# Kernel tuning notes

Measured on AMD Instinct MI355X. Metric: run time of the kernel, lower is better.

## Reference

```python
import jax, jax.numpy as jnp
import numpy as np


def _conv1x1(x, W, b):
    # x: [b,c,h,w], W: [out,in], b: [out]
    return jnp.einsum('oi,bihw->bohw', W, x) + b[None, :, None, None]


def setup_inputs() -> dict:
    key = jax.random.key(0)
    ks = jax.random.split(key, 8)
    B, C, H, W = 4, 256, 64, 64
    s = 1.0 / np.sqrt(C)
    return {
        'x1': jax.random.normal(ks[0], (B, C, H, W), jnp.float32),
        'x2': jax.random.normal(ks[1], (B, C, H, W), jnp.float32),
        'Wq': jax.random.normal(ks[2], (C, C), jnp.float32) * s,
        'bq': jax.random.normal(ks[3], (C,), jnp.float32) * 0.01,
        'Wk': jax.random.normal(ks[4], (C, C), jnp.float32) * s,
        'bk': jax.random.normal(ks[5], (C,), jnp.float32) * 0.01,
        'Wv': jax.random.normal(ks[6], (C, C), jnp.float32) * s,
        'bv': jax.random.normal(ks[7], (C,), jnp.float32) * 0.01,
    }


def reference(x1, x2, Wq, bq, Wk, bk, Wv, bv):
    b, c, h, w = x1.shape
    n = h * w
    q = _conv1x1(x1, Wq, bq).reshape(b, c, n)   # [b,c,n]
    k = _conv1x1(x2, Wk, bk).reshape(b, c, n)   # [b,c,n]
    v = _conv1x1(x2, Wv, bv).reshape(b, c, n)   # [b,c,n]
    # scores[b,i,j] = sum_c q[b,c,i] * k[b,c,j]; softmax over j (last dim)
    scores = jnp.einsum('bci,bcj->bij', q, k)
    attn = jax.nn.softmax(scores, axis=-1)      # [b,n,n]
    # out[b,c,i] = sum_j v[b,c,j] * attn[b,i,j]  (v @ attn^T)
    out = jnp.einsum('bcj,bij->bci', v, attn)
    return out.reshape(b, c, h, w)
```

## Files before the change

### kernel.cpp

```cpp
#include <hip/hip_runtime.h>

#define BATCH 4
#define CDIM 256
#define NDIM 4096
#define SPLITS 4
#define KSPLIT (NDIM / SPLITS)
#define JT 32
#define NTILES (KSPLIT / JT)

typedef unsigned short u16;
typedef unsigned int u32;
typedef _Float16 f16;
typedef __attribute__((ext_vector_type(8))) _Float16 half8;
typedef __attribute__((ext_vector_type(4))) float floatx4;

__device__ __forceinline__ void load_lds_128(const void* g, void* l) {
  __builtin_amdgcn_global_load_lds(
      (const __attribute__((address_space(1))) u32*)g,
      (__attribute__((address_space(3))) u32*)l, 16, 0, 0);
}

__global__ __launch_bounds__(256) void prep_w_k(
    const float* __restrict__ wq, const float* __restrict__ wk,
    const float* __restrict__ wv, f16* __restrict__ whq,
    f16* __restrict__ whk, f16* __restrict__ whv) {
  const int gid = blockIdx.x * 256 + threadIdx.x;
  const int a = gid >> 13;
  const int r = gid & 8191;
  const float* src = (a == 0) ? wq : ((a == 1) ? wk : wv);
  f16* dst = (a == 0) ? whq : ((a == 1) ? whk : whv);
  float4 v0 = *(const float4*)(src + r * 8);
  float4 v1 = *(const float4*)(src + r * 8 + 4);
  half8 h;
  h[0] = (f16)v0.x; h[1] = (f16)v0.y; h[2] = (f16)v0.z; h[3] = (f16)v0.w;
  h[4] = (f16)v1.x; h[5] = (f16)v1.y; h[6] = (f16)v1.z; h[7] = (f16)v1.w;
  *(half8*)(dst + r * 8) = h;
}

__global__ __launch_bounds__(256) void transpose_k(
    const float* __restrict__ x1, const float* __restrict__ x2,
    f16* __restrict__ xt1, f16* __restrict__ xt2) {
  __shared__ __align__(16) float tile[64 * 68];
  const int z = blockIdx.z;
  const float* src = (z & 1) ? x2 : x1;
  f16* dst = (z & 1) ? xt2 : xt1;
  const int b = z >> 1;
  src += (size_t)b * CDIM * NDIM;
  dst += (size_t)b * NDIM * CDIM;
  const int n0 = blockIdx.x * 64, c0 = blockIdx.y * 64;
  const int t = threadIdx.x;
#pragma unroll
  for (int it = 0; it < 4; ++it) {
    int chunk = t + it * 256;
    int row = chunk >> 4;
    int col4 = (chunk & 15) << 2;
    float4 v = *(const float4*)(src + (size_t)(c0 + row) * NDIM + (n0 + col4));
    *(float4*)&tile[row * 68 + col4] = v;
  }
  __syncthreads();
#pragma unroll
  for (int it = 0; it < 2; ++it) {
    int task = t + it * 256;
    int nl = task >> 3;
    int cb = (task & 7) << 3;
    half8 h;
#pragma unroll
    for (int j = 0; j < 8; ++j) h[j] = (f16)tile[(cb + j) * 68 + nl];
    *(half8*)(dst + (size_t)(n0 + nl) * CDIM + (c0 + cb)) = h;
  }
}

__global__ __launch_bounds__(256, 2) void proj_qk_k(
    const f16* __restrict__ xt1, const f16* __restrict__ xt2,
    const f16* __restrict__ whq, const float* __restrict__ bq,
    const f16* __restrict__ whk, const float* __restrict__ bk,
    f16* __restrict__ qt, f16* __restrict__ kt) {
  const int z = blockIdx.z;
  const int which = z & 1, b = z >> 1;
  const f16* xt = which ? xt2 : xt1;
  const f16* w = which ? whk : whq;
  const float* bias = which ? bk : bq;
  f16* outp = which ? kt : qt;
  xt += (size_t)b * NDIM * CDIM;
  outp += (size_t)b * NDIM * CDIM;
  const int c0 = blockIdx.x * 128, i0 = blockIdx.y * 128;
  const int tid = threadIdx.x;
  const int wave = tid >> 6, lane = tid & 63, l16 = lane & 15, grp = lane >> 4;
  const int wi = (wave & 1) * 64, wc = (wave >> 1) * 64;
  floatx4 acc[4][4];
#pragma unroll
  for (int mb = 0; mb < 4; ++mb)
#pragma unroll
    for (int nb = 0; nb < 4; ++nb) acc[mb][nb] = (floatx4){0.f, 0.f, 0.f, 0.f};
#pragma unroll
  for (int ks = 0; ks < 8; ++ks) {
    const int kofs = ks * 32 + grp * 8;
    half8 a[4], bb[4];
#pragma unroll
    for (int mb = 0; mb < 4; ++mb)
      a[mb] = *(const half8*)(xt + (size_t)(i0 + wi + mb * 16 + l16) * CDIM + kofs);
#pragma unroll
    for (int nb = 0; nb < 4; ++nb)
      bb[nb] = *(const half8*)(w + (size_t)(c0 + wc + nb * 16 + l16) * CDIM + kofs);
#pragma unroll
    for (int mb = 0; mb < 4; ++mb)
#pragma unroll
      for (int nb = 0; nb < 4; ++nb)
        acc[mb][nb] = __builtin_amdgcn_mfma_f32_16x16x32_f16(a[mb], bb[nb], acc[mb][nb], 0, 0, 0);
  }
#pragma unroll
  for (int nb = 0; nb < 4; ++nb) {
    const int c = c0 + wc + nb * 16 + l16;
    const float bv = bias[c];
#pragma unroll
    for (int mb = 0; mb < 4; ++mb) {
      const int ibase = i0 + wi + mb * 16 + grp * 4;
#pragma unroll
      for (int r = 0; r < 4; ++r)
        outp[(size_t)(ibase + r) * CDIM + c] = (f16)(acc[mb][nb][r] + bv);
    }
  }
}

__global__ __launch_bounds__(256, 2) void proj_v_k(
    const f16* __restrict__ xt2, const f16* __restrict__ whv,
    const float* __restrict__ bv, f16* __restrict__ vsout) {
  const int b = blockIdx.z;
  const f16* xt = xt2 + (size_t)b * NDIM * CDIM;
  f16* outp = vsout + (size_t)b * CDIM * NDIM;
  const int c0 = blockIdx.x * 128, j0 = blockIdx.y * 128;
  const int tid = threadIdx.x;
  const int wave = tid >> 6, lane = tid & 63, l16 = lane & 15, grp = lane >> 4;
  const int wc = (wave & 1) * 64, wj = (wave >> 1) * 64;
  floatx4 acc[4][4];
#pragma unroll
  for (int mb = 0; mb < 4; ++mb)
#pragma unroll
    for (int nb = 0; nb < 4; ++nb) acc[mb][nb] = (floatx4){0.f, 0.f, 0.f, 0.f};
#pragma unroll
  for (int ks = 0; ks < 8; ++ks) {
    const int kofs = ks * 32 + grp * 8;
    half8 a[4], bb[4];
#pragma unroll
    for (int mb = 0; mb < 4; ++mb)
      a[mb] = *(const half8*)(whv + (size_t)(c0 + wc + mb * 16 + l16) * CDIM + kofs);
#pragma unroll
    for (int nb = 0; nb < 4; ++nb)
      bb[nb] = *(const half8*)(xt + (size_t)(j0 + wj + nb * 16 + l16) * CDIM + kofs);
#pragma unroll
    for (int mb = 0; mb < 4; ++mb)
#pragma unroll
      for (int nb = 0; nb < 4; ++nb)
        acc[mb][nb] = __builtin_amdgcn_mfma_f32_16x16x32_f16(a[mb], bb[nb], acc[mb][nb], 0, 0, 0);
  }
#pragma unroll
  for (int mb = 0; mb < 4; ++mb)
#pragma unroll
    for (int r = 0; r < 4; ++r) {
      const int c = c0 + wc + mb * 16 + grp * 4 + r;
      const float bvv = bv[c];
#pragma unroll
      for (int nb = 0; nb < 4; ++nb) {
        const int j = j0 + wj + nb * 16 + l16;
        outp[(size_t)c * NDIM + j] = (f16)(acc[mb][nb][r] + bvv);
      }
    }
}

__global__ __launch_bounds__(256, 2) void flash_k(
    const f16* __restrict__ qt, const f16* __restrict__ kt,
    const f16* __restrict__ vs, f16* __restrict__ pO,
    float* __restrict__ pm, float* __restrict__ pl) {
  __shared__ __align__(16) u16 smem[25600];
  const int bx = blockIdx.x;
  const int c16 = bx & 15;
  const int b = c16 >> 2, s = c16 & 3;
  const int i0 = (bx >> 4) * 128;
  const int jwin = s * KSPLIT;
  const f16* Q = qt + (size_t)b * NDIM * CDIM;
  const f16* K = kt + (size_t)b * NDIM * CDIM;
  const f16* V = vs + (size_t)b * CDIM * NDIM;
  const int tid = threadIdx.x;
  const int wave = tid >> 6, lane = tid & 63, l16 = lane & 15, grp = lane >> 4;
  u16* bK = smem;
  u16* bV = smem + 8192;
  float* Pw = (float*)(smem + 16384) + wave * (32 * 36);

  half8 qf[2][8];
#pragma unroll
  for (int mb = 0; mb < 2; ++mb)
#pragma unroll
    for (int ks = 0; ks < 8; ++ks)
      qf[mb][ks] = *(const half8*)(Q + (size_t)(i0 + wave * 32 + mb * 16 + l16) * CDIM +
                                   ks * 32 + grp * 8);

  floatx4 O[2][16];
#pragma unroll
  for (int mb = 0; mb < 2; ++mb)
#pragma unroll
    for (int cb = 0; cb < 16; ++cb) O[mb][cb] = (floatx4){0.f, 0.f, 0.f, 0.f};
  float m_[2][4], l_[2][4];
#pragma unroll
  for (int mb = 0; mb < 2; ++mb)
#pragma unroll
    for (int r = 0; r < 4; ++r) { m_[mb][r] = -1e30f; l_[mb][r] = 0.f; }

  for (int tt = 0; tt < NTILES; ++tt) {
    const int j0 = jwin + tt * JT;
    __syncthreads();
#pragma unroll
    for (int it = 0; it < 4; ++it) {
      const int row = wave * 8 + it * 2 + (lane >> 5);
      const int p = lane & 31;
      const int g = p ^ (row & 7);
      load_lds_128(K + (size_t)(j0 + row) * CDIM + g * 8, &bK[(wave * 8 + it * 2) * 256]);
    }
#pragma unroll
    for (int it = 0; it < 4; ++it) {
      const int c = wave * 64 + it * 16 + (lane >> 2);
      const int p = lane & 3;
      const int g = p ^ (c & 3);
      load_lds_128(V + (size_t)c * NDIM + j0 + g * 8, &bV[(wave * 64 + it * 16) * 32]);
    }
    __syncthreads();

    floatx4 S[2][2];
#pragma unroll
    for (int mb = 0; mb < 2; ++mb)
#pragma unroll
      for (int jb = 0; jb < 2; ++jb) S[mb][jb] = (floatx4){0.f, 0.f, 0.f, 0.f};
#pragma unroll
    for (int ks = 0; ks < 8; ++ks) {
      const int chunk = ks * 4 + grp;
#pragma unroll
      for (int jb = 0; jb < 2; ++jb) {
        const int row = jb * 16 + l16;
        half8 kf = *(const half8*)&bK[row * 256 + ((chunk ^ (row & 7)) << 3)];
        S[0][jb] = __builtin_amdgcn_mfma_f32_16x16x32_f16(qf[0][ks], kf, S[0][jb], 0, 0, 0);
        S[1][jb] = __builtin_amdgcn_mfma_f32_16x16x32_f16(qf[1][ks], kf, S[1][jb], 0, 0, 0);
      }
    }

#pragma unroll
    for (int mb = 0; mb < 2; ++mb) {
      float mnew[4];
#pragma unroll
      for (int r = 0; r < 4; ++r) mnew[r] = fmaxf(S[mb][0][r], S[mb][1][r]);
#pragma unroll
      for (int mask = 1; mask < 16; mask <<= 1)
#pragma unroll
        for (int r = 0; r < 4; ++r) mnew[r] = fmaxf(mnew[r], __shfl_xor(mnew[r], mask, 64));
      float alpha[4], rs[4];
#pragma unroll
      for (int r = 0; r < 4; ++r) {
        const float mt = fmaxf(m_[mb][r], mnew[r]);
        alpha[r] = __expf(m_[mb][r] - mt);
        m_[mb][r] = mt;
      }
#pragma unroll
      for (int r = 0; r < 4; ++r) {
        S[mb][0][r] = __expf(S[mb][0][r] - m_[mb][r]);
        S[mb][1][r] = __expf(S[mb][1][r] - m_[mb][r]);
        rs[r] = S[mb][0][r] + S[mb][1][r];
      }
#pragma unroll
      for (int mask = 1; mask < 16; mask <<= 1)
#pragma unroll
        for (int r = 0; r < 4; ++r) rs[r] += __shfl_xor(rs[r], mask, 64);
#pragma unroll
      for (int r = 0; r < 4; ++r) l_[mb][r] = l_[mb][r] * alpha[r] + rs[r];
#pragma unroll
      for (int cb = 0; cb < 16; ++cb)
#pragma unroll
        for (int r = 0; r < 4; ++r) O[mb][cb][r] *= alpha[r];
    }

#pragma unroll
    for (int mb = 0; mb < 2; ++mb)
#pragma unroll
      for (int jb = 0; jb < 2; ++jb)
#pragma unroll
        for (int r = 0; r < 4; ++r)
          Pw[(mb * 16 + grp * 4 + r) * 36 + jb * 16 + l16] = S[mb][jb][r];
    half8 pa[2];
#pragma unroll
    for (int mb = 0; mb < 2; ++mb) {
      floatx4 u0 = *(const floatx4*)&Pw[(mb * 16 + l16) * 36 + grp * 8];
      floatx4 u1 = *(const floatx4*)&Pw[(mb * 16 + l16) * 36 + grp * 8 + 4];
      half8 h;
      h[0] = (f16)u0[0]; h[1] = (f16)u0[1]; h[2] = (f16)u0[2]; h[3] = (f16)u0[3];
      h[4] = (f16)u1[0]; h[5] = (f16)u1[1]; h[6] = (f16)u1[2]; h[7] = (f16)u1[3];
      pa[mb] = h;
    }

#pragma unroll
    for (int cb = 0; cb < 16; ++cb) {
      const int c = cb * 16 + l16;
      half8 vf = *(const half8*)&bV[c * 32 + ((grp ^ (c & 3)) << 3)];
      O[0][cb] = __builtin_amdgcn_mfma_f32_16x16x32_f16(pa[0], vf, O[0][cb], 0, 0, 0);
      O[1][cb] = __builtin_amdgcn_mfma_f32_16x16x32_f16(pa[1], vf, O[1][cb], 0, 0, 0);
    }
  }

#pragma unroll
  for (int quarter = 0; quarter < 4; ++quarter) {
    __syncthreads();
    float* sO = (float*)smem;
#pragma unroll
    for (int mb = 0; mb < 2; ++mb)
#pragma unroll
      for (int cb4 = 0; cb4 < 4; ++cb4) {
        const int cb = quarter * 4 + cb4;
        const int cl = cb4 * 16 + l16;
        const int i = wave * 32 + mb * 16 + grp * 4;
        *(floatx4*)&sO[cl * 132 + i] = O[mb][cb];
      }
    __syncthreads();
    const size_t obase = ((size_t)(b * SPLITS + s) * CDIM + quarter * 64) * NDIM + i0;
#pragma unroll
    for (int it = 0; it < 4; ++it) {
      const int task = tid + it * 256;
      const int cl = task >> 4, p = (task & 15) * 8;
      floatx4 v0 = *(const floatx4*)&sO[cl * 132 + p];
      floatx4 v1 = *(const floatx4*)&sO[cl * 132 + p + 4];
      half8 h;
      h[0] = (f16)v0[0]; h[1] = (f16)v0[1]; h[2] = (f16)v0[2]; h[3] = (f16)v0[3];
      h[4] = (f16)v1[0]; h[5] = (f16)v1[1]; h[6] = (f16)v1[2]; h[7] = (f16)v1[3];
      *(half8*)(pO + obase + (size_t)cl * NDIM + p) = h;
    }
  }
  if (l16 == 0) {
    const int base = (b * SPLITS + s) * NDIM + i0;
#pragma unroll
    for (int mb = 0; mb < 2; ++mb)
#pragma unroll
      for (int r = 0; r < 4; ++r) {
        const int i = wave * 32 + mb * 16 + grp * 4 + r;
        pm[base + i] = m_[mb][r];
        pl[base + i] = l_[mb][r];
      }
  }
}

__global__ __launch_bounds__(256) void combine_k(
    const f16* __restrict__ pO, const float* __restrict__ pm,
    const float* __restrict__ pl, float* __restrict__ out) {
  __shared__ float su[SPLITS][64];
  const int b = blockIdx.x >> 6;
  const int i0 = (blockIdx.x & 63) * 64;
  const int t = threadIdx.x;
  if (t < 64) {
    const int i = i0 + t;
    float mv[SPLITS], w[SPLITS];
    float M = -3e38f;
#pragma unroll
    for (int s = 0; s < SPLITS; ++s) {
      mv[s] = pm[(b * SPLITS + s) * NDIM + i];
      M = fmaxf(M, mv[s]);
    }
    float L = 0.f;
#pragma unroll
    for (int s = 0; s < SPLITS; ++s) {
      w[s] = __expf(mv[s] - M);
      L += pl[(b * SPLITS + s) * NDIM + i] * w[s];
    }
    const float invL = 1.0f / L;
#pragma unroll
    for (int s = 0; s < SPLITS; ++s) su[s][t] = w[s] * invL;
  }
  __syncthreads();
#pragma unroll
  for (int it = 0; it < 8; ++it) {
    const int task = t + it * 256;
    const int c = task >> 3, p = (task & 7) * 8;
    float acc[8] = {0.f, 0.f, 0.f, 0.f, 0.f, 0.f, 0.f, 0.f};
#pragma unroll
    for (int s = 0; s < SPLITS; ++s) {
      const f16* src = pO + ((size_t)(b * SPLITS + s) * CDIM + c) * NDIM + i0 + p;
      half8 h = *(const half8*)src;
#pragma unroll
      for (int j = 0; j < 8; ++j) acc[j] += su[s][p + j] * (float)h[j];
    }
    float* dst = out + ((size_t)b * CDIM + c) * NDIM + i0 + p;
    float4 lo = {acc[0], acc[1], acc[2], acc[3]};
    float4 hi = {acc[4], acc[5], acc[6], acc[7]};
    *(float4*)dst = lo;
    *(float4*)(dst + 4) = hi;
  }
}

extern "C" void kernel_launch(void* const* d_in, const int* in_sizes, int n_in,
                              void* d_out, int out_size, void* d_ws, size_t ws_size,
                              hipStream_t stream) {
  const float* x1 = (const float*)d_in[0];
  const float* x2 = (const float*)d_in[1];
  const float* Wq = (const float*)d_in[2];
  const float* bq = (const float*)d_in[3];
  const float* Wk = (const float*)d_in[4];
  const float* bk = (const float*)d_in[5];
  const float* Wv = (const float*)d_in[6];
  const float* bv = (const float*)d_in[7];
  float* out = (float*)d_out;
  char* ws = (char*)d_ws;
  f16* qtp = (f16*)(ws + 0);
  f16* ktp = (f16*)(ws + 8388608);
  f16* vsp = (f16*)(ws + 16777216);
  f16* xt1 = (f16*)(ws + 25165824);
  f16* xt2 = (f16*)(ws + 33554432);
  f16* whq = (f16*)(ws + 41943040);
  f16* whk = whq + CDIM * CDIM;
  f16* whv = whk + CDIM * CDIM;
  f16* pO = (f16*)(ws + 25165824);
  float* pm = (float*)(ws + 58720256);
  float* pl = (float*)(ws + 58982400);

  prep_w_k<<<dim3(96), dim3(256), 0, stream>>>(Wq, Wk, Wv, whq, whk, whv);
  transpose_k<<<dim3(NDIM / 64, CDIM / 64, 2 * BATCH), dim3(256), 0, stream>>>(x1, x2, xt1, xt2);
  proj_qk_k<<<dim3(2, 32, 2 * BATCH), dim3(256), 0, stream>>>(xt1, xt2, whq, bq, whk, bk, qtp, ktp);
  proj_v_k<<<dim3(2, 32, BATCH), dim3(256), 0, stream>>>(xt2, whv, bv, vsp);
  flash_k<<<dim3(512), dim3(256), 0, stream>>>(qtp, ktp, vsp, pO, pm, pl);
  combine_k<<<dim3(256), dim3(256), 0, stream>>>(pO, pm, pl, out);
}
```

Before: 310.3 us.

## Enlarge flash query tile, double-buffer K/V loads, defer row-sum reduction

The flash kernel now handles 256 query rows per block (64 per wave), so each K/V tile staged in LDS is reused across twice as many rows, and the grid is halved to 256 blocks at one block per CU. K/V tiles are double-buffered, with the next tile's async global-to-LDS load issued before computing on the current one, removing one barrier per iteration. Q fragments are no longer held in registers and are reloaded from global memory each tile. The softmax row-sum shuffle reduction is deferred to after the loop, and O rescaling is skipped when no row maximum increases. The costs are higher register pressure, lower occupancy, and repeated Q traffic through cache.

```diff
diff --git a/kernel.cpp b/kernel.cpp
--- a/kernel.cpp
+++ b/kernel.cpp
@@ -167,82 +167,94 @@
     }
 }
 
-__global__ __launch_bounds__(256, 2) void flash_k(
+__global__ __launch_bounds__(256, 1) void flash_k(
     const f16* __restrict__ qt, const f16* __restrict__ kt,
     const f16* __restrict__ vs, f16* __restrict__ pO,
     float* __restrict__ pm, float* __restrict__ pl) {
-  __shared__ __align__(16) u16 smem[25600];
+  __shared__ __align__(16) u16 smem[51200];
   const int bx = blockIdx.x;
   const int c16 = bx & 15;
   const int b = c16 >> 2, s = c16 & 3;
-  const int i0 = (bx >> 4) * 128;
+  const int i0 = (bx >> 4) * 256;
   const int jwin = s * KSPLIT;
-  const f16* Q = qt + (size_t)b * NDIM * CDIM;
   const f16* K = kt + (size_t)b * NDIM * CDIM;
   const f16* V = vs + (size_t)b * CDIM * NDIM;
   const int tid = threadIdx.x;
   const int wave = tid >> 6, lane = tid & 63, l16 = lane & 15, grp = lane >> 4;
-  u16* bK = smem;
-  u16* bV = smem + 8192;
-  float* Pw = (float*)(smem + 16384) + wave * (32 * 36);
-
-  half8 qf[2][8];
-#pragma unroll
-  for (int mb = 0; mb < 2; ++mb)
-#pragma unroll
-    for (int ks = 0; ks < 8; ++ks)
-      qf[mb][ks] = *(const half8*)(Q + (size_t)(i0 + wave * 32 + mb * 16 + l16) * CDIM +
-                                   ks * 32 + grp * 8);
-
-  floatx4 O[2][16];
-#pragma unroll
-  for (int mb = 0; mb < 2; ++mb)
+  const int wq = wave * 64;
+  const f16* Qw = qt + (size_t)b * NDIM * CDIM + (size_t)(i0 + wq + l16) * CDIM + grp * 8;
+
+  float* Pw = (float*)(smem + 32768) + wave * (64 * 36);
+
+  floatx4 O[4][16];
+#pragma unroll
+  for (int mb = 0; mb < 4; ++mb)
 #pragma unroll
     for (int cb = 0; cb < 16; ++cb) O[mb][cb] = (floatx4){0.f, 0.f, 0.f, 0.f};
-  float m_[2][4], l_[2][4];
-#pragma unroll
-  for (int mb = 0; mb < 2; ++mb)
-#pragma unroll
-    for (int r = 0; r < 4; ++r) { m_[mb][r] = -1e30f; l_[mb][r] = 0.f; }
+  float m_[4][4], lsum[4][4];
+#pragma unroll
+  for (int mb = 0; mb < 4; ++mb)
+#pragma unroll
+    for (int r = 0; r < 4; ++r) { m_[mb][r] = -1e30f; lsum[mb][r] = 0.f; }
+
+  const int kr2 = lane >> 5, kp = lane & 31;
+  const int vrow = lane >> 2, vp = lane & 3;
+
+#define STAGE(J0, BUF)                                                         \
+  {                                                                            \
+    u16* sK = smem + (BUF) * 16384;                                            \
+    u16* sV = sK + 8192;                                                       \
+    _Pragma("unroll") for (int it = 0; it < 4; ++it) {                         \
+      const int row = wave * 8 + it * 2 + kr2;                                 \
+      const int g = kp ^ (row & 7);                                            \
+      load_lds_128(K + (size_t)((J0) + row) * CDIM + g * 8,                    \
+                   &sK[(wave * 8 + it * 2) * 256]);                            \
+    }                                                                          \
+    _Pragma("unroll") for (int it = 0; it < 4; ++it) {                         \
+      const int c = wave * 64 + it * 16 + vrow;                                \
+      const int g = vp ^ ((c >> 2) & 3);                                       \
+      load_lds_128(V + (size_t)c * NDIM + (J0) + g * 8,                        \
+                   &sV[(wave * 64 + it * 16) * 32]);                           \
+    }                                                                          \
+  }
+
+  STAGE(jwin, 0)
 
   for (int tt = 0; tt < NTILES; ++tt) {
-    const int j0 = jwin + tt * JT;
+    u16* bK = smem + (tt & 1) * 16384;
+    u16* bV = bK + 8192;
     __syncthreads();
-#pragma unroll
-    for (int it = 0; it < 4; ++it) {
-      const int row = wave * 8 + it * 2 + (lane >> 5);
-      const int p = lane & 31;
-      const int g = p ^ (row & 7);
-      load_lds_128(K + (size_t)(j0 + row) * CDIM + g * 8, &bK[(wave * 8 + it * 2) * 256]);
-    }
-#pragma unroll
-    for (int it = 0; it < 4; ++it) {
-      const int c = wave * 64 + it * 16 + (lane >> 2);
-      const int p = lane & 3;
-      const int g = p ^ (c & 3);
-      load_lds_128(V + (size_t)c * NDIM + j0 + g * 8, &bV[(wave * 64 + it * 16) * 32]);
-    }
-    __syncthreads();
-
-    floatx4 S[2][2];
-#pragma unroll
-    for (int mb = 0; mb < 2; ++mb)
+    if (tt + 1 < NTILES) STAGE(jwin + (tt + 1) * JT, (tt + 1) & 1)
+
+    floatx4 S[4][2];
+#pragma unroll
+    for (int mb = 0; mb < 4; ++mb)
 #pragma unroll
       for (int jb = 0; jb < 2; ++jb) S[mb][jb] = (floatx4){0.f, 0.f, 0.f, 0.f};
 #pragma unroll
-    for (int ks = 0; ks < 8; ++ks) {
-      const int chunk = ks * 4 + grp;
-#pragma unroll
-      for (int jb = 0; jb < 2; ++jb) {
-        const int row = jb * 16 + l16;
-        half8 kf = *(const half8*)&bK[row * 256 + ((chunk ^ (row & 7)) << 3)];
-        S[0][jb] = __builtin_amdgcn_mfma_f32_16x16x32_f16(qf[0][ks], kf, S[0][jb], 0, 0, 0);
-        S[1][jb] = __builtin_amdgcn_mfma_f32_16x16x32_f16(qf[1][ks], kf, S[1][jb], 0, 0, 0);
-      }
-    }
-
-#pragma unroll
-    for (int mb = 0; mb < 2; ++mb) {
+    for (int half = 0; half < 2; ++half) {
+      half8 qh[4][4];
+#pragma unroll
+      for (int mb = 0; mb < 4; ++mb)
+#pragma unroll
+        for (int kk = 0; kk < 4; ++kk)
+          qh[mb][kk] = *(const half8*)(Qw + (size_t)(mb * 16) * CDIM + (half * 4 + kk) * 32);
+#pragma unroll
+      for (int kk = 0; kk < 4; ++kk) {
+        const int chunk = (half * 4 + kk) * 4 + grp;
+#pragma unroll
+        for (int jb = 0; jb < 2; ++jb) {
+          const int row = jb * 16 + l16;
+          half8 kf = *(const half8*)&bK[row * 256 + ((chunk ^ (row & 7)) << 3)];
+#pragma unroll
+          for (int mb = 0; mb < 4; ++mb)
+            S[mb][jb] = __builtin_amdgcn_mfma_f32_16x16x32_f16(qh[mb][kk], kf, S[mb][jb], 0, 0, 0);
+        }
+      }
+    }
+
+#pragma unroll
+    for (int mb = 0; mb < 4; ++mb) {
       float mnew[4];
 #pragma unroll
       for (int r = 0; r < 4; ++r) mnew[r] = fmaxf(S[mb][0][r], S[mb][1][r]);
@@ -250,41 +262,39 @@
       for (int mask = 1; mask < 16; mask <<= 1)
 #pragma unroll
         for (int r = 0; r < 4; ++r) mnew[r] = fmaxf(mnew[r], __shfl_xor(mnew[r], mask, 64));
-      float alpha[4], rs[4];
-#pragma unroll
-      for (int r = 0; r < 4; ++r) {
-        const float mt = fmaxf(m_[mb][r], mnew[r]);
-        alpha[r] = __expf(m_[mb][r] - mt);
-        m_[mb][r] = mt;
+      bool upd = false;
+#pragma unroll
+      for (int r = 0; r < 4; ++r) upd = upd || (mnew[r] > m_[mb][r]);
+      if (__any(upd)) {
+        float alpha[4];
+#pragma unroll
+        for (int r = 0; r < 4; ++r) {
+          const float mt = fmaxf(m_[mb][r], mnew[r]);
+          alpha[r] = __expf(m_[mb][r] - mt);
+          m_[mb][r] = mt;
+          lsum[mb][r] *= alpha[r];
+        }
+#pragma unroll
+        for (int cb = 0; cb < 16; ++cb)
+#pragma unroll
+          for (int r = 0; r < 4; ++r) O[mb][cb][r] *= alpha[r];
       }
 #pragma unroll
       for (int r = 0; r < 4; ++r) {
         S[mb][0][r] = __expf(S[mb][0][r] - m_[mb][r]);
         S[mb][1][r] = __expf(S[mb][1][r] - m_[mb][r]);
-        rs[r] = S[mb][0][r] + S[mb][1][r];
-      }
-#pragma unroll
-      for (int mask = 1; mask < 16; mask <<= 1)
-#pragma unroll
-        for (int r = 0; r < 4; ++r) rs[r] += __shfl_xor(rs[r], mask, 64);
-#pragma unroll
-      for (int r = 0; r < 4; ++r) l_[mb][r] = l_[mb][r] * alpha[r] + rs[r];
-#pragma unroll
-      for (int cb = 0; cb < 16; ++cb)
-#pragma unroll
-        for (int r = 0; r < 4; ++r) O[mb][cb][r] *= alpha[r];
-    }
-
-#pragma unroll
-    for (int mb = 0; mb < 2; ++mb)
+        lsum[mb][r] += S[mb][0][r] + S[mb][1][r];
+      }
 #pragma unroll
       for (int jb = 0; jb < 2; ++jb)
 #pragma unroll
         for (int r = 0; r < 4; ++r)
           Pw[(mb * 16 + grp * 4 + r) * 36 + jb * 16 + l16] = S[mb][jb][r];
-    half8 pa[2];
-#pragma unroll
-    for (int mb = 0; mb < 2; ++mb) {
+    }
+
+    half8 pa[4];
+#pragma unroll
+    for (int mb = 0; mb < 4; ++mb) {
       floatx4 u0 = *(const floatx4*)&Pw[(mb * 16 + l16) * 36 + grp * 8];
       floatx4 u1 = *(const floatx4*)&Pw[(mb * 16 + l16) * 36 + grp * 8 + 4];
       half8 h;
@@ -296,10 +306,29 @@
 #pragma unroll
     for (int cb = 0; cb < 16; ++cb) {
       const int c = cb * 16 + l16;
-      half8 vf = *(const half8*)&bV[c * 32 + ((grp ^ (c & 3)) << 3)];
-      O[0][cb] = __builtin_amdgcn_mfma_f32_16x16x32_f16(pa[0], vf, O[0][cb], 0, 0, 0);
-      O[1][cb] = __builtin_amdgcn_mfma_f32_16x16x32_f16(pa[1], vf, O[1][cb], 0, 0, 0);
-    }
+      half8 vf = *(const half8*)&bV[c * 32 + ((grp ^ ((c >> 2) & 3)) << 3)];
+#pragma unroll
+      for (int mb = 0; mb < 4; ++mb)
+        O[mb][cb] = __builtin_amdgcn_mfma_f32_16x16x32_f16(pa[mb], vf, O[mb][cb], 0, 0, 0);
+    }
+  }
+
+#pragma unroll
+  for (int mask = 1; mask < 16; mask <<= 1)
+#pragma unroll
+    for (int mb = 0; mb < 4; ++mb)
+#pragma unroll
+      for (int r = 0; r < 4; ++r) lsum[mb][r] += __shfl_xor(lsum[mb][r], mask, 64);
+  if (l16 == 0) {
+    const int base = (b * SPLITS + s) * NDIM + i0;
+#pragma unroll
+    for (int mb = 0; mb < 4; ++mb)
+#pragma unroll
+      for (int r = 0; r < 4; ++r) {
+        const int i = wq + mb * 16 + grp * 4 + r;
+        pm[base + i] = m_[mb][r];
+        pl[base + i] = lsum[mb][r];
+      }
   }
 
 #pragma unroll
@@ -307,38 +336,27 @@
     __syncthreads();
     float* sO = (float*)smem;
 #pragma unroll
-    for (int mb = 0; mb < 2; ++mb)
+    for (int mb = 0; mb < 4; ++mb)
 #pragma unroll
       for (int cb4 = 0; cb4 < 4; ++cb4) {
         const int cb = quarter * 4 + cb4;
         const int cl = cb4 * 16 + l16;
-        const int i = wave * 32 + mb * 16 + grp * 4;
-        *(floatx4*)&sO[cl * 132 + i] = O[mb][cb];
+        const int i = wq + mb * 16 + grp * 4;
+        *(floatx4*)&sO[cl * 260 + i] = O[mb][cb];
       }
     __syncthreads();
     const size_t obase = ((size_t)(b * SPLITS + s) * CDIM + quarter * 64) * NDIM + i0;
 #pragma unroll
-    for (int it = 0; it < 4; ++it) {
+    for (int it = 0; it < 8; ++it) {
       const int task = tid + it * 256;
-      const int cl = task >> 4, p = (task & 15) * 8;
-      floatx4 v0 = *(const floatx4*)&sO[cl * 132 + p];
-      floatx4 v1 = *(const floatx4*)&sO[cl * 132 + p + 4];
+      const int cl = task >> 5, p = (task & 31) * 8;
+      floatx4 v0 = *(const floatx4*)&sO[cl * 260 + p];
+      floatx4 v1 = *(const floatx4*)&sO[cl * 260 + p + 4];
       half8 h;
       h[0] = (f16)v0[0]; h[1] = (f16)v0[1]; h[2] = (f16)v0[2]; h[3] = (f16)v0[3];
       h[4] = (f16)v1[0]; h[5] = (f16)v1[1]; h[6] = (f16)v1[2]; h[7] = (f16)v1[3];
       *(half8*)(pO + obase + (size_t)cl * NDIM + p) = h;
     }
-  }
-  if (l16 == 0) {
-    const int base = (b * SPLITS + s) * NDIM + i0;
-#pragma unroll
-    for (int mb = 0; mb < 2; ++mb)
-#pragma unroll
-      for (int r = 0; r < 4; ++r) {
-        const int i = wave * 32 + mb * 16 + grp * 4 + r;
-        pm[base + i] = m_[mb][r];
-        pl[base + i] = l_[mb][r];
-      }
   }
 }
 
@@ -418,6 +436,6 @@
   transpose_k<<<dim3(NDIM / 64, CDIM / 64, 2 * BATCH), dim3(256), 0, stream>>>(x1, x2, xt1, xt2);
   proj_qk_k<<<dim3(2, 32, 2 * BATCH), dim3(256), 0, stream>>>(xt1, xt2, whq, bq, whk, bk, qtp, ktp);
   proj_v_k<<<dim3(2, 32, BATCH), dim3(256), 0, stream>>>(xt2, whv, bv, vsp);
-  flash_k<<<dim3(512), dim3(256), 0, stream>>>(qtp, ktp, vsp, pO, pm, pl);
+  flash_k<<<dim3(256), dim3(256), 0, stream>>>(qtp, ktp, vsp, pO, pm, pl);
   combine_k<<<dim3(256), dim3(256), 0, stream>>>(pO, pm, pl, out);
 }
```

Result: slower. 707.3 us (+127.9%).

## Double-buffer K/V tiles and transpose PV MFMA for row-local softmax

Applied to the files above, without the earlier changes.

Splits LDS into two K/V buffers so the next tile's global-to-LDS loads are issued while the current tile is computed, leaving one barrier per iteration. Swaps the MFMA operands in the P·V product so each lane holds a full query row. This lets the online softmax use per-lane max and sum with only two cross-lane shuffles, and the O rescale is skipped when no alpha in the wave is below one. The LDS-staged epilogue is replaced with direct strided f16 stores, which are less coalesced. LDS use per block also grows.

```diff
diff --git a/kernel.cpp b/kernel.cpp
--- a/kernel.cpp
+++ b/kernel.cpp
@@ -171,7 +171,7 @@
     const f16* __restrict__ qt, const f16* __restrict__ kt,
     const f16* __restrict__ vs, f16* __restrict__ pO,
     float* __restrict__ pm, float* __restrict__ pl) {
-  __shared__ __align__(16) u16 smem[25600];
+  __shared__ __align__(16) u16 smem[32768 + 4608];
   const int bx = blockIdx.x;
   const int c16 = bx & 15;
   const int b = c16 >> 2, s = c16 & 3;
@@ -182,9 +182,7 @@
   const f16* V = vs + (size_t)b * CDIM * NDIM;
   const int tid = threadIdx.x;
   const int wave = tid >> 6, lane = tid & 63, l16 = lane & 15, grp = lane >> 4;
-  u16* bK = smem;
-  u16* bV = smem + 8192;
-  float* Pw = (float*)(smem + 16384) + wave * (32 * 36);
+  float* Pw = (float*)(smem + 32768) + wave * (16 * 36);
 
   half8 qf[2][8];
 #pragma unroll
@@ -199,30 +197,37 @@
   for (int mb = 0; mb < 2; ++mb)
 #pragma unroll
     for (int cb = 0; cb < 16; ++cb) O[mb][cb] = (floatx4){0.f, 0.f, 0.f, 0.f};
-  float m_[2][4], l_[2][4];
-#pragma unroll
-  for (int mb = 0; mb < 2; ++mb)
-#pragma unroll
-    for (int r = 0; r < 4; ++r) { m_[mb][r] = -1e30f; l_[mb][r] = 0.f; }
+  float m_[2] = {-1e30f, -1e30f};
+  float lsum[2] = {0.f, 0.f};
+
+  const int kr2 = lane >> 5, kp = lane & 31;
+  const int vrow = lane >> 2, vp = lane & 3;
+
+#define STAGE(J0, BUF)                                                         \
+  {                                                                            \
+    u16* sK = smem + (BUF) * 16384;                                            \
+    u16* sV = sK + 8192;                                                       \
+    _Pragma("unroll") for (int it = 0; it < 4; ++it) {                         \
+      const int row = wave * 8 + it * 2 + kr2;                                 \
+      const int g = kp ^ (row & 7);                                            \
+      load_lds_128(K + (size_t)((J0) + row) * CDIM + g * 8,                    \
+                   &sK[(wave * 8 + it * 2) * 256]);                            \
+    }                                                                          \
+    _Pragma("unroll") for (int it = 0; it < 4; ++it) {                         \
+      const int c = wave * 64 + it * 16 + vrow;                                \
+      const int g = vp ^ ((c >> 2) & 3);                                       \
+      load_lds_128(V + (size_t)c * NDIM + (J0) + g * 8,                        \
+                   &sV[(wave * 64 + it * 16) * 32]);                           \
+    }                                                                          \
+  }
+
+  STAGE(jwin, 0)
 
   for (int tt = 0; tt < NTILES; ++tt) {
-    const int j0 = jwin + tt * JT;
     __syncthreads();
-#pragma unroll
-    for (int it = 0; it < 4; ++it) {
-      const int row = wave * 8 + it * 2 + (lane >> 5);
-      const int p = lane & 31;
-      const int g = p ^ (row & 7);
-      load_lds_128(K + (size_t)(j0 + row) * CDIM + g * 8, &bK[(wave * 8 + it * 2) * 256]);
-    }
-#pragma unroll
-    for (int it = 0; it < 4; ++it) {
-      const int c = wave * 64 + it * 16 + (lane >> 2);
-      const int p = lane & 3;
-      const int g = p ^ (c & 3);
-      load_lds_128(V + (size_t)c * NDIM + j0 + g * 8, &bV[(wave * 64 + it * 16) * 32]);
-    }
-    __syncthreads();
+    if (tt + 1 < NTILES) STAGE(jwin + (tt + 1) * JT, (tt + 1) & 1)
+    u16* bK = smem + (tt & 1) * 16384;
+    u16* bV = bK + 8192;
 
     floatx4 S[2][2];
 #pragma unroll
@@ -241,104 +246,80 @@
       }
     }
 
+    float alpha[2];
+    half8 pa[2];
 #pragma unroll
     for (int mb = 0; mb < 2; ++mb) {
-      float mnew[4];
-#pragma unroll
-      for (int r = 0; r < 4; ++r) mnew[r] = fmaxf(S[mb][0][r], S[mb][1][r]);
-#pragma unroll
-      for (int mask = 1; mask < 16; mask <<= 1)
-#pragma unroll
-        for (int r = 0; r < 4; ++r) mnew[r] = fmaxf(mnew[r], __shfl_xor(mnew[r], mask, 64));
-      float alpha[4], rs[4];
-#pragma unroll
-      for (int r = 0; r < 4; ++r) {
-        const float mt = fmaxf(m_[mb][r], mnew[r]);
-        alpha[r] = __expf(m_[mb][r] - mt);
-        m_[mb][r] = mt;
-      }
-#pragma unroll
-      for (int r = 0; r < 4; ++r) {
-        S[mb][0][r] = __expf(S[mb][0][r] - m_[mb][r]);
-        S[mb][1][r] = __expf(S[mb][1][r] - m_[mb][r]);
-        rs[r] = S[mb][0][r] + S[mb][1][r];
-      }
-#pragma unroll
-      for (int mask = 1; mask < 16; mask <<= 1)
-#pragma unroll
-        for (int r = 0; r < 4; ++r) rs[r] += __shfl_xor(rs[r], mask, 64);
-#pragma unroll
-      for (int r = 0; r < 4; ++r) l_[mb][r] = l_[mb][r] * alpha[r] + rs[r];
-#pragma unroll
-      for (int cb = 0; cb < 16; ++cb)
-#pragma unroll
-        for (int r = 0; r < 4; ++r) O[mb][cb][r] *= alpha[r];
-    }
-
-#pragma unroll
-    for (int mb = 0; mb < 2; ++mb)
 #pragma unroll
       for (int jb = 0; jb < 2; ++jb)
 #pragma unroll
         for (int r = 0; r < 4; ++r)
-          Pw[(mb * 16 + grp * 4 + r) * 36 + jb * 16 + l16] = S[mb][jb][r];
-    half8 pa[2];
-#pragma unroll
-    for (int mb = 0; mb < 2; ++mb) {
-      floatx4 u0 = *(const floatx4*)&Pw[(mb * 16 + l16) * 36 + grp * 8];
-      floatx4 u1 = *(const floatx4*)&Pw[(mb * 16 + l16) * 36 + grp * 8 + 4];
+          Pw[(grp * 4 + r) * 36 + jb * 16 + l16] = S[mb][jb][r];
+      floatx4 u0 = *(const floatx4*)&Pw[l16 * 36 + grp * 8];
+      floatx4 u1 = *(const floatx4*)&Pw[l16 * 36 + grp * 8 + 4];
+      float mx = fmaxf(fmaxf(fmaxf(u0[0], u0[1]), fmaxf(u0[2], u0[3])),
+                       fmaxf(fmaxf(u1[0], u1[1]), fmaxf(u1[2], u1[3])));
+      mx = fmaxf(mx, __shfl_xor(mx, 16, 64));
+      mx = fmaxf(mx, __shfl_xor(mx, 32, 64));
+      const float mnew = fmaxf(m_[mb], mx);
+      alpha[mb] = __expf(m_[mb] - mnew);
+      m_[mb] = mnew;
+      float pe[8];
+#pragma unroll
+      for (int j = 0; j < 4; ++j) pe[j] = __expf(u0[j] - mnew);
+#pragma unroll
+      for (int j = 0; j < 4; ++j) pe[4 + j] = __expf(u1[j] - mnew);
+      const float ps = ((pe[0] + pe[1]) + (pe[2] + pe[3])) +
+                       ((pe[4] + pe[5]) + (pe[6] + pe[7]));
+      lsum[mb] = lsum[mb] * alpha[mb] + ps;
       half8 h;
-      h[0] = (f16)u0[0]; h[1] = (f16)u0[1]; h[2] = (f16)u0[2]; h[3] = (f16)u0[3];
-      h[4] = (f16)u1[0]; h[5] = (f16)u1[1]; h[6] = (f16)u1[2]; h[7] = (f16)u1[3];
+#pragma unroll
+      for (int j = 0; j < 8; ++j) h[j] = (f16)pe[j];
       pa[mb] = h;
+    }
+
+    if (__any(alpha[0] < 1.f) || __any(alpha[1] < 1.f)) {
+#pragma unroll
+      for (int mb = 0; mb < 2; ++mb)
+#pragma unroll
+        for (int cb = 0; cb < 16; ++cb) O[mb][cb] *= alpha[mb];
     }
 
 #pragma unroll
     for (int cb = 0; cb < 16; ++cb) {
       const int c = cb * 16 + l16;
-      half8 vf = *(const half8*)&bV[c * 32 + ((grp ^ (c & 3)) << 3)];
-      O[0][cb] = __builtin_amdgcn_mfma_f32_16x16x32_f16(pa[0], vf, O[0][cb], 0, 0, 0);
-      O[1][cb] = __builtin_amdgcn_mfma_f32_16x16x32_f16(pa[1], vf, O[1][cb], 0, 0, 0);
-    }
-  }
-
-#pragma unroll
-  for (int quarter = 0; quarter < 4; ++quarter) {
-    __syncthreads();
-    float* sO = (float*)smem;
-#pragma unroll
-    for (int mb = 0; mb < 2; ++mb)
-#pragma unroll
-      for (int cb4 = 0; cb4 < 4; ++cb4) {
-        const int cb = quarter * 4 + cb4;
-        const int cl = cb4 * 16 + l16;
-        const int i = wave * 32 + mb * 16 + grp * 4;
-        *(floatx4*)&sO[cl * 132 + i] = O[mb][cb];
-      }
-    __syncthreads();
-    const size_t obase = ((size_t)(b * SPLITS + s) * CDIM + quarter * 64) * NDIM + i0;
-#pragma unroll
-    for (int it = 0; it < 4; ++it) {
-      const int task = tid + it * 256;
-      const int cl = task >> 4, p = (task & 15) * 8;
-      floatx4 v0 = *(const floatx4*)&sO[cl * 132 + p];
-      floatx4 v1 = *(const floatx4*)&sO[cl * 132 + p + 4];
-      half8 h;
-      h[0] = (f16)v0[0]; h[1] = (f16)v0[1]; h[2] = (f16)v0[2]; h[3] = (f16)v0[3];
-      h[4] = (f16)v1[0]; h[5] = (f16)v1[1]; h[6] = (f16)v1[2]; h[7] = (f16)v1[3];
-      *(half8*)(pO + obase + (size_t)cl * NDIM + p) = h;
-    }
-  }
-  if (l16 == 0) {
+      half8 vf = *(const half8*)&bV[c * 32 + ((grp ^ ((c >> 2) & 3)) << 3)];
+      O[0][cb] = __builtin_amdgcn_mfma_f32_16x16x32_f16(vf, pa[0], O[0][cb], 0, 0, 0);
+      O[1][cb] = __builtin_amdgcn_mfma_f32_16x16x32_f16(vf, pa[1], O[1][cb], 0, 0, 0);
+    }
+  }
+
+#pragma unroll
+  for (int mb = 0; mb < 2; ++mb) {
+    lsum[mb] += __shfl_xor(lsum[mb], 16, 64);
+    lsum[mb] += __shfl_xor(lsum[mb], 32, 64);
+  }
+  if (grp == 0) {
     const int base = (b * SPLITS + s) * NDIM + i0;
 #pragma unroll
-    for (int mb = 0; mb < 2; ++mb)
-#pragma unroll
-      for (int r = 0; r < 4; ++r) {
-        const int i = wave * 32 + mb * 16 + grp * 4 + r;
-        pm[base + i] = m_[mb][r];
-        pl[base + i] = l_[mb][r];
-      }
+    for (int mb = 0; mb < 2; ++mb) {
+      const int i = wave * 32 + mb * 16 + l16;
+      pm[base + i] = m_[mb];
+      pl[base + i] = lsum[mb];
+    }
+  }
+
+  const size_t pbase = (size_t)(b * SPLITS + s) * CDIM * NDIM;
+#pragma unroll
+  for (int mb = 0; mb < 2; ++mb) {
+    const int i = i0 + wave * 32 + mb * 16 + l16;
+#pragma unroll
+    for (int cb = 0; cb < 16; ++cb) {
+      const int c = cb * 16 + grp * 4;
+#pragma unroll
+      for (int r = 0; r < 4; ++r)
+        pO[pbase + (size_t)(c + r) * NDIM + i] = (f16)O[mb][cb][r];
+    }
   }
 }
 
```

Result: faster. 261.9 us (-15.6%).
